# Kernel tuning notes

Hardware: AMD Instinct MI355X
Metric: run time of the kernel (lower is better)

Reference implementation:

```python
import jax, jax.numpy as jnp
import numpy as np


def _windowed_attn(q, k, v, window_size, num_heads):
    # q, k, v: [B, T, D] with T % window_size == 0
    B, T, D = q.shape
    hd = D // num_heads
    scale = 1.0 / np.sqrt(hd).astype(np.float32)
    nw = T // window_size
    # [B, nw, w, H, hd]
    qh = q.reshape(B, nw, window_size, num_heads, hd)
    kh = k.reshape(B, nw, window_size, num_heads, hd)
    vh = v.reshape(B, nw, window_size, num_heads, hd)
    # attention scores per window: [B, nw, H, w, w]
    attn = jnp.einsum('bnqhd,bnkhd->bnhqk', qh, kh) * scale
    attn = jax.nn.softmax(attn, axis=-1)
    out = jnp.einsum('bnhqk,bnkhd->bnqhd', attn, vh)
    return out.reshape(B, T, D)


def setup_inputs() -> dict:
    key = jax.random.key(0)
    ks = jax.random.split(key, 6)
    B, D = 8, 512
    T1, T2 = 4096, 2048
    return {
        'q1': jax.random.normal(ks[0], (B, T1, D), dtype=jnp.float32),
        'k1': jax.random.normal(ks[1], (B, T1, D), dtype=jnp.float32),
        'v1': jax.random.normal(ks[2], (B, T1, D), dtype=jnp.float32),
        'q2': jax.random.normal(ks[3], (B, T2, D), dtype=jnp.float32),
        'k2': jax.random.normal(ks[4], (B, T2, D), dtype=jnp.float32),
        'v2': jax.random.normal(ks[5], (B, T2, D), dtype=jnp.float32),
        'window_size': 128,
        'num_heads': 8,
    }


def reference(q1, k1, v1, q2, k2, v2, window_size, num_heads):
    out1 = _windowed_attn(q1, k1, v1, window_size, num_heads)
    out2 = _windowed_attn(q2, k2, v2, window_size, num_heads)
    return (out1, out2)
```

## Files before the change

kernel.cpp:

```cpp
#include <hip/hip_runtime.h>
#include <hip/hip_bf16.h>

typedef __attribute__((ext_vector_type(4))) float f32x4;
typedef __attribute__((ext_vector_type(8))) short bf16x8;
typedef __attribute__((ext_vector_type(4))) unsigned short u16x4;

#define NH 8
#define HD 64
#define WSZ 128
#define DM 512

__device__ __forceinline__ unsigned short f2bf(float f) {
    unsigned int u = __float_as_uint(f);
    u += 0x7fffu + ((u >> 16) & 1u);
    return (unsigned short)(u >> 16);
}

__global__ __launch_bounds__(256, 2) void wattn_kernel(
    const float* __restrict__ q1, const float* __restrict__ k1,
    const float* __restrict__ v1, float* __restrict__ o1, int nw1,
    const float* __restrict__ q2, const float* __restrict__ k2,
    const float* __restrict__ v2, float* __restrict__ o2, int nw2,
    int nblk1)
{
    __shared__ __align__(16) unsigned short Kl[128][72];
    __shared__ __align__(16) unsigned short Vt[64][128];
    __shared__ __align__(16) unsigned short Pl[4][32][40];

    const int t = threadIdx.x;
    const int lane = t & 63;
    const int wid = t >> 6;
    const int g = lane >> 4;
    const int c = lane & 15;

    int bid = blockIdx.x;
    const float *q, *k, *v; float* o; int nw;
    if (bid < nblk1) { q = q1; k = k1; v = v1; o = o1; nw = nw1; }
    else { bid -= nblk1; q = q2; k = k2; v = v2; o = o2; nw = nw2; }

    const int h = bid & (NH - 1);
    const int w = (bid / NH) % nw;
    const int b = bid / (NH * nw);

    const size_t row0 = ((size_t)b * nw + w) * WSZ;
    const float* Qp = q + row0 * DM + h * HD;
    const float* Kp = k + row0 * DM + h * HD;
    const float* Vp = v + row0 * DM + h * HD;
    float* Op = o + row0 * DM + h * HD;

#pragma unroll
    for (int i = 0; i < 8; ++i) {
        int e = (i * 256 + t) * 4;
        int kr = e >> 6;
        int dc = e & 63;
        f32x4 kv = *reinterpret_cast<const f32x4*>(Kp + (size_t)kr * DM + dc);
        u16x4 kb;
        kb[0] = f2bf(kv[0]); kb[1] = f2bf(kv[1]);
        kb[2] = f2bf(kv[2]); kb[3] = f2bf(kv[3]);
        *reinterpret_cast<u16x4*>(&Kl[kr][dc]) = kb;

        f32x4 vv = *reinterpret_cast<const f32x4*>(Vp + (size_t)kr * DM + dc);
#pragma unroll
        for (int j = 0; j < 4; ++j) {
            int d = dc + j;
            int xk = kr ^ (((d >> 1) & 7) << 3);
            Vt[d][xk] = f2bf(vv[j]);
        }
    }

    const int qrow0 = wid * 32;
    bf16x8 qf[2][2];
#pragma unroll
    for (int m = 0; m < 2; ++m) {
#pragma unroll
        for (int ks = 0; ks < 2; ++ks) {
            const float* src = Qp + (size_t)(qrow0 + m * 16 + c) * DM + ks * 32 + g * 8;
            f32x4 a = *reinterpret_cast<const f32x4*>(src);
            f32x4 bq = *reinterpret_cast<const f32x4*>(src + 4);
            bf16x8 f;
            f[0] = (short)f2bf(a[0]);  f[1] = (short)f2bf(a[1]);
            f[2] = (short)f2bf(a[2]);  f[3] = (short)f2bf(a[3]);
            f[4] = (short)f2bf(bq[0]); f[5] = (short)f2bf(bq[1]);
            f[6] = (short)f2bf(bq[2]); f[7] = (short)f2bf(bq[3]);
            qf[m][ks] = f;
        }
    }

    __syncthreads();

    f32x4 acc[2][8] = {};
#pragma unroll
    for (int ks = 0; ks < 2; ++ks) {
#pragma unroll
        for (int n = 0; n < 8; ++n) {
            bf16x8 kf = *reinterpret_cast<const bf16x8*>(&Kl[n * 16 + c][ks * 32 + g * 8]);
            acc[0][n] = __builtin_amdgcn_mfma_f32_16x16x32_bf16(qf[0][ks], kf, acc[0][n], 0, 0, 0);
            acc[1][n] = __builtin_amdgcn_mfma_f32_16x16x32_bf16(qf[1][ks], kf, acc[1][n], 0, 0, 0);
        }
    }

    float rinv[2][4];
#pragma unroll
    for (int m = 0; m < 2; ++m) {
#pragma unroll
        for (int r = 0; r < 4; ++r) {
            float mx = acc[m][0][r];
#pragma unroll
            for (int n = 1; n < 8; ++n) mx = fmaxf(mx, acc[m][n][r]);
#pragma unroll
            for (int off = 1; off < 16; off <<= 1) mx = fmaxf(mx, __shfl_xor(mx, off));
            float s = 0.f;
#pragma unroll
            for (int n = 0; n < 8; ++n) {
                float p = __expf(0.125f * (acc[m][n][r] - mx));
                acc[m][n][r] = p;
                s += p;
            }
#pragma unroll
            for (int off = 1; off < 16; off <<= 1) s += __shfl_xor(s, off);
            rinv[m][r] = 1.0f / s;
        }
    }

    f32x4 oacc[2][4] = {};
#pragma unroll
    for (int ck = 0; ck < 4; ++ck) {
#pragma unroll
        for (int m = 0; m < 2; ++m) {
#pragma unroll
            for (int nn = 0; nn < 2; ++nn) {
#pragma unroll
                for (int r = 0; r < 4; ++r) {
                    float p = acc[m][ck * 2 + nn][r] * rinv[m][r];
                    Pl[wid][m * 16 + g * 4 + r][nn * 16 + c] = f2bf(p);
                }
            }
        }
        bf16x8 pf0 = *reinterpret_cast<const bf16x8*>(&Pl[wid][c][g * 8]);
        bf16x8 pf1 = *reinterpret_cast<const bf16x8*>(&Pl[wid][16 + c][g * 8]);
#pragma unroll
        for (int n = 0; n < 4; ++n) {
            int d = n * 16 + c;
            int xk = (ck * 32 + g * 8) ^ (((d >> 1) & 7) << 3);
            bf16x8 vf = *reinterpret_cast<const bf16x8*>(&Vt[d][xk]);
            oacc[0][n] = __builtin_amdgcn_mfma_f32_16x16x32_bf16(pf0, vf, oacc[0][n], 0, 0, 0);
            oacc[1][n] = __builtin_amdgcn_mfma_f32_16x16x32_bf16(pf1, vf, oacc[1][n], 0, 0, 0);
        }
    }

#pragma unroll
    for (int m = 0; m < 2; ++m) {
#pragma unroll
        for (int n = 0; n < 4; ++n) {
#pragma unroll
            for (int r = 0; r < 4; ++r) {
                int row = qrow0 + m * 16 + g * 4 + r;
                Op[(size_t)row * DM + n * 16 + c] = oacc[m][n][r];
            }
        }
    }
}

extern "C" void kernel_launch(void* const* d_in, const int* in_sizes, int n_in,
                              void* d_out, int out_size, void* d_ws, size_t ws_size,
                              hipStream_t stream) {
    const float* q1 = (const float*)d_in[0];
    const float* k1 = (const float*)d_in[1];
    const float* v1 = (const float*)d_in[2];
    const float* q2 = (const float*)d_in[3];
    const float* k2 = (const float*)d_in[4];
    const float* v2 = (const float*)d_in[5];

    const int B = 8;
    const int nw1 = in_sizes[0] / (B * DM * WSZ);
    const int nw2 = in_sizes[3] / (B * DM * WSZ);

    float* o1 = (float*)d_out;
    float* o2 = o1 + (size_t)in_sizes[0];

    const int nblk1 = B * nw1 * NH;
    const int nblk2 = B * nw2 * NH;

    wattn_kernel<<<dim3(nblk1 + nblk2), dim3(256), 0, stream>>>(
        q1, k1, v1, o1, nw1, q2, k2, v2, o2, nw2, nblk1);
}
```

Before: 91.39 us.

## Load K fragments directly from global, drop K LDS tile, defer softmax normalization

K is now read straight from global memory into MFMA operand registers instead of being staged through a shared-memory tile. Each wave re-reads all of K, but LDS use drops enough to allow 4 blocks per CU instead of 2. Softmax normalization is moved to the output store, and exp uses exp2 with a folded constant. Packed bf16 conversion and an XOR swizzle on the P tile aim to cut conversion ALU work and LDS bank conflicts. V and Q loads are issued up front to overlap global latency, at the cost of more registers under the tighter occupancy bound.

```diff
diff --git a/kernel.cpp b/kernel.cpp
--- a/kernel.cpp
+++ b/kernel.cpp
@@ -3,27 +3,34 @@
 
 typedef __attribute__((ext_vector_type(4))) float f32x4;
 typedef __attribute__((ext_vector_type(8))) short bf16x8;
-typedef __attribute__((ext_vector_type(4))) unsigned short u16x4;
 
 #define NH 8
 #define HD 64
 #define WSZ 128
 #define DM 512
 
-__device__ __forceinline__ unsigned short f2bf(float f) {
-    unsigned int u = __float_as_uint(f);
-    u += 0x7fffu + ((u >> 16) & 1u);
-    return (unsigned short)(u >> 16);
-}
-
-__global__ __launch_bounds__(256, 2) void wattn_kernel(
+__device__ __forceinline__ unsigned int pk2bf(float lo, float hi) {
+    union { __hip_bfloat162 h; unsigned int u; } r;
+    r.h = __float22bfloat162_rn(make_float2(lo, hi));
+    return r.u;
+}
+
+__device__ __forceinline__ bf16x8 pack8(f32x4 a, f32x4 b) {
+    union { unsigned int u[4]; bf16x8 v; } r;
+    r.u[0] = pk2bf(a[0], a[1]);
+    r.u[1] = pk2bf(a[2], a[3]);
+    r.u[2] = pk2bf(b[0], b[1]);
+    r.u[3] = pk2bf(b[2], b[3]);
+    return r.v;
+}
+
+__global__ __launch_bounds__(256, 4) void wattn_kernel(
     const float* __restrict__ q1, const float* __restrict__ k1,
     const float* __restrict__ v1, float* __restrict__ o1, int nw1,
     const float* __restrict__ q2, const float* __restrict__ k2,
     const float* __restrict__ v2, float* __restrict__ o2, int nw2,
     int nblk1)
 {
-    __shared__ __align__(16) unsigned short Kl[128][72];
     __shared__ __align__(16) unsigned short Vt[64][128];
     __shared__ __align__(16) unsigned short Pl[4][32][40];
 
@@ -48,60 +55,68 @@
     const float* Vp = v + row0 * DM + h * HD;
     float* Op = o + row0 * DM + h * HD;
 
+    f32x4 vv[8];
 #pragma unroll
     for (int i = 0; i < 8; ++i) {
         int e = (i * 256 + t) * 4;
-        int kr = e >> 6;
-        int dc = e & 63;
-        f32x4 kv = *reinterpret_cast<const f32x4*>(Kp + (size_t)kr * DM + dc);
-        u16x4 kb;
-        kb[0] = f2bf(kv[0]); kb[1] = f2bf(kv[1]);
-        kb[2] = f2bf(kv[2]); kb[3] = f2bf(kv[3]);
-        *reinterpret_cast<u16x4*>(&Kl[kr][dc]) = kb;
-
-        f32x4 vv = *reinterpret_cast<const f32x4*>(Vp + (size_t)kr * DM + dc);
+        int kr = e >> 6, dc = e & 63;
+        vv[i] = *reinterpret_cast<const f32x4*>(Vp + (size_t)kr * DM + dc);
+    }
+
+    const int qrow0 = wid * 32;
+    f32x4 qa[2][2], qb[2][2];
+#pragma unroll
+    for (int m = 0; m < 2; ++m)
+#pragma unroll
+        for (int ks = 0; ks < 2; ++ks) {
+            const float* src = Qp + (size_t)(qrow0 + m * 16 + c) * DM + ks * 32 + g * 8;
+            qa[m][ks] = *reinterpret_cast<const f32x4*>(src);
+            qb[m][ks] = *reinterpret_cast<const f32x4*>(src + 4);
+        }
+
+#pragma unroll
+    for (int i = 0; i < 8; ++i) {
+        int e = (i * 256 + t) * 4;
+        int kr = e >> 6, dc = e & 63;
 #pragma unroll
         for (int j = 0; j < 4; ++j) {
             int d = dc + j;
             int xk = kr ^ (((d >> 1) & 7) << 3);
-            Vt[d][xk] = f2bf(vv[j]);
-        }
-    }
-
-    const int qrow0 = wid * 32;
+            union { __hip_bfloat16 h; unsigned short u; } cv;
+            cv.h = __float2bfloat16(vv[i][j]);
+            Vt[d][xk] = cv.u;
+        }
+    }
+
     bf16x8 qf[2][2];
 #pragma unroll
-    for (int m = 0; m < 2; ++m) {
-#pragma unroll
-        for (int ks = 0; ks < 2; ++ks) {
-            const float* src = Qp + (size_t)(qrow0 + m * 16 + c) * DM + ks * 32 + g * 8;
+    for (int m = 0; m < 2; ++m)
+#pragma unroll
+        for (int ks = 0; ks < 2; ++ks)
+            qf[m][ks] = pack8(qa[m][ks], qb[m][ks]);
+
+    f32x4 acc[2][8] = {};
+#pragma unroll
+    for (int ks = 0; ks < 2; ++ks) {
+        bf16x8 kf[8];
+#pragma unroll
+        for (int n = 0; n < 8; ++n) {
+            const float* src = Kp + (size_t)(n * 16 + c) * DM + ks * 32 + g * 8;
             f32x4 a = *reinterpret_cast<const f32x4*>(src);
             f32x4 bq = *reinterpret_cast<const f32x4*>(src + 4);
-            bf16x8 f;
-            f[0] = (short)f2bf(a[0]);  f[1] = (short)f2bf(a[1]);
-            f[2] = (short)f2bf(a[2]);  f[3] = (short)f2bf(a[3]);
-            f[4] = (short)f2bf(bq[0]); f[5] = (short)f2bf(bq[1]);
-            f[6] = (short)f2bf(bq[2]); f[7] = (short)f2bf(bq[3]);
-            qf[m][ks] = f;
-        }
-    }
-
-    __syncthreads();
-
-    f32x4 acc[2][8] = {};
-#pragma unroll
-    for (int ks = 0; ks < 2; ++ks) {
+            kf[n] = pack8(a, bq);
+        }
 #pragma unroll
         for (int n = 0; n < 8; ++n) {
-            bf16x8 kf = *reinterpret_cast<const bf16x8*>(&Kl[n * 16 + c][ks * 32 + g * 8]);
-            acc[0][n] = __builtin_amdgcn_mfma_f32_16x16x32_bf16(qf[0][ks], kf, acc[0][n], 0, 0, 0);
-            acc[1][n] = __builtin_amdgcn_mfma_f32_16x16x32_bf16(qf[1][ks], kf, acc[1][n], 0, 0, 0);
-        }
-    }
-
+            acc[0][n] = __builtin_amdgcn_mfma_f32_16x16x32_bf16(qf[0][ks], kf[n], acc[0][n], 0, 0, 0);
+            acc[1][n] = __builtin_amdgcn_mfma_f32_16x16x32_bf16(qf[1][ks], kf[n], acc[1][n], 0, 0, 0);
+        }
+    }
+
+    const float CEXP = 0.125f * 1.4426950408889634f;
     float rinv[2][4];
 #pragma unroll
-    for (int m = 0; m < 2; ++m) {
+    for (int m = 0; m < 2; ++m)
 #pragma unroll
         for (int r = 0; r < 4; ++r) {
             float mx = acc[m][0][r];
@@ -112,7 +127,7 @@
             float s = 0.f;
 #pragma unroll
             for (int n = 0; n < 8; ++n) {
-                float p = __expf(0.125f * (acc[m][n][r] - mx));
+                float p = exp2f((acc[m][n][r] - mx) * CEXP);
                 acc[m][n][r] = p;
                 s += p;
             }
@@ -120,24 +135,27 @@
             for (int off = 1; off < 16; off <<= 1) s += __shfl_xor(s, off);
             rinv[m][r] = 1.0f / s;
         }
-    }
+
+    __syncthreads();
 
     f32x4 oacc[2][4] = {};
 #pragma unroll
     for (int ck = 0; ck < 4; ++ck) {
 #pragma unroll
         for (int m = 0; m < 2; ++m) {
-#pragma unroll
-            for (int nn = 0; nn < 2; ++nn) {
-#pragma unroll
-                for (int r = 0; r < 4; ++r) {
-                    float p = acc[m][ck * 2 + nn][r] * rinv[m][r];
-                    Pl[wid][m * 16 + g * 4 + r][nn * 16 + c] = f2bf(p);
-                }
+            const int rowb = m * 16 + g * 4;
+            const int cl0 = c ^ (g << 3);
+            const int cl1 = (16 + c) ^ (g << 3);
+#pragma unroll
+            for (int r = 0; r < 4; ++r) {
+                unsigned int pr = pk2bf(acc[m][ck * 2][r], acc[m][ck * 2 + 1][r]);
+                Pl[wid][rowb + r][cl0] = (unsigned short)(pr & 0xffffu);
+                Pl[wid][rowb + r][cl1] = (unsigned short)(pr >> 16);
             }
         }
-        bf16x8 pf0 = *reinterpret_cast<const bf16x8*>(&Pl[wid][c][g * 8]);
-        bf16x8 pf1 = *reinterpret_cast<const bf16x8*>(&Pl[wid][16 + c][g * 8]);
+        const int rb = (g ^ ((c >> 2) & 3)) * 8;
+        bf16x8 pf0 = *reinterpret_cast<const bf16x8*>(&Pl[wid][c][rb]);
+        bf16x8 pf1 = *reinterpret_cast<const bf16x8*>(&Pl[wid][16 + c][rb]);
 #pragma unroll
         for (int n = 0; n < 4; ++n) {
             int d = n * 16 + c;
@@ -149,16 +167,14 @@
     }
 
 #pragma unroll
-    for (int m = 0; m < 2; ++m) {
-#pragma unroll
-        for (int n = 0; n < 4; ++n) {
+    for (int m = 0; m < 2; ++m)
+#pragma unroll
+        for (int n = 0; n < 4; ++n)
 #pragma unroll
             for (int r = 0; r < 4; ++r) {
                 int row = qrow0 + m * 16 + g * 4 + r;
-                Op[(size_t)row * DM + n * 16 + c] = oacc[m][n][r];
+                Op[(size_t)row * DM + n * 16 + c] = oacc[m][n][r] * rinv[m][r];
             }
-        }
-    }
 }
 
 extern "C" void kernel_launch(void* const* d_in, const int* in_sizes, int n_in,
```

After: 114.0 us. +24.7%, slower.
